# Optimization experiments

Hardware: AMD Instinct MI355X
Metric: run time of the kernel (lower is better)

The kernel has to match this reference:

```python
import math
import jax, jax.numpy as jnp
import numpy as np

NUM_HEAD = 16

def get_slopes(n):
    def pow2(n):
        start = 2 ** (-2 ** (-(math.log2(n) - 3)))
        return [start * start ** i for i in range(n)]
    if math.log2(n).is_integer():
        return pow2(n)
    c = 2 ** math.floor(math.log2(n))
    return pow2(c) + get_slopes(2 * c)[0::2][: n - c]

def setup_inputs() -> dict:
    key = jax.random.key(0)
    ks = jax.random.split(key, 9)
    B, T, C = 2, 2048, 2048
    x = jax.random.normal(ks[0], (B, T, C), dtype=jnp.float32)
    std = 0.02
    Wq = std * jax.random.normal(ks[1], (C, C), dtype=jnp.float32)
    Wk = std * jax.random.normal(ks[2], (C, C), dtype=jnp.float32)
    Wv = std * jax.random.normal(ks[3], (C, C), dtype=jnp.float32)
    Wo = (0.02 / np.sqrt(2 * 24)) * jax.random.normal(ks[4], (C, C), dtype=jnp.float32)
    bq = jnp.zeros((C,), jnp.float32)
    bk = jnp.zeros((C,), jnp.float32)
    bv = jnp.zeros((C,), jnp.float32)
    bo = jnp.zeros((C,), jnp.float32)
    return {"x": x, "Wq": Wq, "bq": bq, "Wk": Wk, "bk": bk,
            "Wv": Wv, "bv": bv, "Wo": Wo, "bo": bo}

def reference(x, Wq, bq, Wk, bk, Wv, bv, Wo, bo):
    B, T, C = x.shape
    H = NUM_HEAD
    D = C // H
    slopes = jnp.asarray(get_slopes(H), dtype=jnp.float32)  # [H]

    def split_heads(y):  # [B,T,C] -> [B,H,T,D]
        return y.reshape(B, T, H, D).transpose(0, 2, 1, 3)

    q = split_heads(x @ Wq + bq)
    k = split_heads(x @ Wk + bk)
    v = split_heads(x @ Wv + bv)

    attn = jnp.einsum("bhqd,bhkd->bhqk", q, k) / jnp.sqrt(jnp.float32(D))
    # ALiBi: bias[h, j] = slopes[h] * (j - (T-1)), broadcast over queries
    alibi = slopes[:, None, None] * (jnp.arange(T, dtype=jnp.float32) - (T - 1))[None, None, :]
    attn = attn + alibi  # [B,H,T,T] + [H,1,T]

    causal = jnp.tril(jnp.ones((T, T), dtype=bool))[None, None]
    attn = jnp.where(causal, attn, jnp.finfo(jnp.float32).min)
    p = jax.nn.softmax(attn, axis=-1)

    o = jnp.einsum("bhqk,bhkd->bhqd", p, v).transpose(0, 2, 1, 3).reshape(B, T, C)
    return o @ Wo + bo
```

## Files before the change

### kernel.cpp

```cpp
#include <hip/hip_runtime.h>
#include <math.h>


typedef unsigned short u16;
using bf16x8 = __attribute__((ext_vector_type(8))) short;
using f32x4  = __attribute__((ext_vector_type(4))) float;

__device__ __forceinline__ u16 f2bf(float f) {
  union { float f; unsigned u; } c; c.f = f;
  unsigned r = c.u + 0x7fffu + ((c.u >> 16) & 1u);
  return (u16)(r >> 16);
}
__device__ __forceinline__ float bf2f(u16 b) {
  union { unsigned u; float f; } c; c.u = ((unsigned)b) << 16; return c.f;
}
__device__ __forceinline__ unsigned cvtpk(float a, float b) {
  unsigned r;
  asm("v_cvt_pk_bf16_f32 %0, %1, %2" : "=v"(r) : "v"(a), "v"(b));
  return r;
}
__device__ __forceinline__ void g2l16(const void* g, void* l) {
  __builtin_amdgcn_global_load_lds(
      (const __attribute__((address_space(1))) void*)g,
      (__attribute__((address_space(3))) void*)l, 16, 0, 0);
}

__device__ __forceinline__ int band_jmin(int s, float slope2) {
  const int idist = (int)(36.0f / slope2);
  const int cut = 64 * s - idist - 31;
  return (cut > 0) ? (cut >> 5) : 0;
}

__device__ const unsigned char uord[48] = {
  15, 16, 32, 17, 33, 14, 18, 34, 19, 35,
  13, 20, 36, 21, 37, 12, 22, 38, 23, 39,
  11, 24, 40, 25, 41, 10, 26, 42, 27, 43,
   9, 28, 44, 29, 45,  8, 30, 46, 31, 47,
   7,  6,  5,  4,  3,  2,  1,  0};

__global__ __launch_bounds__(256) void split_f32(const float* __restrict__ in,
                                                 u16* __restrict__ hi, int n4) {
  for (int i = blockIdx.x * 256 + threadIdx.x; i < n4; i += gridDim.x * 256) {
    const float4 v = ((const float4*)in)[i];
    ushort4 h;
    h.x = f2bf(v.x); h.y = f2bf(v.y); h.z = f2bf(v.z); h.w = f2bf(v.w);
    ((ushort4*)hi)[i] = h;
  }
}

__global__ __launch_bounds__(256) void tsplit4_f32(
    const float* __restrict__ W0, const float* __restrict__ W1,
    const float* __restrict__ W2, const float* __restrict__ W3,
    u16* __restrict__ D0, u16* __restrict__ D1,
    u16* __restrict__ D2, u16* __restrict__ D3,
    int N, int K, float sc0) {
  __shared__ float tile[64][68];
  const int z = blockIdx.z;
  const float* W = (z == 0) ? W0 : (z == 1) ? W1 : (z == 2) ? W2 : W3;
  u16* Wth = (z == 0) ? D0 : (z == 1) ? D1 : (z == 2) ? D2 : D3;
  const float sc = (z == 0) ? sc0 : 1.f;
  const int tid = threadIdx.x;
  const int k0 = blockIdx.y * 64, n0 = blockIdx.x * 64;
  const int rr = tid >> 4, cc = (tid & 15) * 4;
#pragma unroll
  for (int u = 0; u < 4; ++u) {
    const float4 v = *(const float4*)&W[(size_t)(k0 + rr + 16 * u) * N + n0 + cc];
    tile[rr + 16 * u][cc + 0] = v.x;
    tile[rr + 16 * u][cc + 1] = v.y;
    tile[rr + 16 * u][cc + 2] = v.z;
    tile[rr + 16 * u][cc + 3] = v.w;
  }
  __syncthreads();
#pragma unroll
  for (int u = 0; u < 4; ++u) {
    const int nn = rr + 16 * u;
    ushort4 h;
    h.x = f2bf(tile[cc + 0][nn] * sc);
    h.y = f2bf(tile[cc + 1][nn] * sc);
    h.z = f2bf(tile[cc + 2][nn] * sc);
    h.w = f2bf(tile[cc + 3][nn] * sc);
    *(ushort4*)&Wth[(size_t)(n0 + nn) * K + k0 + cc] = h;
  }
}

template <int MODE>
__global__ __launch_bounds__(512, 4) void gemm256x128(
    const u16* __restrict__ Ah, const u16* __restrict__ Bth,
    const float* __restrict__ bias, const float* __restrict__ bias2,
    float bsc, u16* __restrict__ outH, u16* __restrict__ outH2,
    float* __restrict__ outF, int MM, int NN, int KK) {
  __shared__ u16 LA[3][8192];
  __shared__ u16 LB[3][4096];

  const int tid = threadIdx.x;
  const int wave = tid >> 6, lane = tid & 63;
  const int g = lane >> 4, q15 = lane & 15;
  const int wr = wave >> 1, wc = wave & 1;
  const int m0 = blockIdx.y * 256, n0 = blockIdx.x * 128;
  const int NT = KK >> 5;
  const int sxg = ((g ^ ((q15 >> 1) & 3)) << 4);

  f32x4 acc[4][4];
#pragma unroll
  for (int f = 0; f < 4; ++f)
#pragma unroll
    for (int j = 0; j < 4; ++j) acc[f][j] = (f32x4){0.f, 0.f, 0.f, 0.f};

  auto stageA = [&](int t, int rbuf) {
#pragma unroll
    for (int l = 0; l < 2; ++l) {
      const int ch = l * 512 + tid;
      const int row = ch >> 2, slot = ch & 3;
      const size_t ga = (size_t)(m0 + row) * KK + t * 32 +
                        ((slot ^ ((row >> 1) & 3)) * 8);
      g2l16(Ah + ga, (char*)(LA[rbuf]) + ch * 16);
    }
  };
  auto stageB = [&](int t, int rbuf) {
    const int ch = tid;
    const int row = ch >> 2, slot = ch & 3;
    const size_t gb = (size_t)(n0 + row) * KK + t * 32 +
                      ((slot ^ ((row >> 1) & 3)) * 8);
    g2l16(Bth + gb, (char*)(LB[rbuf]) + ch * 16);
  };

  stageA(0, 0); stageB(0, 0);
  __builtin_amdgcn_sched_barrier(0);
  if (NT > 1) { stageA(1, 1); stageB(1, 1); }
  __builtin_amdgcn_sched_barrier(0);
  if (NT > 1) { asm volatile("s_waitcnt vmcnt(3)" ::: "memory"); }
  else        { asm volatile("s_waitcnt vmcnt(0)" ::: "memory"); }
  __builtin_amdgcn_sched_barrier(0);
  __builtin_amdgcn_s_barrier();

  int rb = 0, rb2 = 2;
  for (int t = 0; t < NT; ++t) {
    const char* baseA = (const char*)(LA[rb]);
    const char* baseB = (const char*)(LB[rb]);

    bf16x8 af[4], bf[4];
#pragma unroll
    for (int f = 0; f < 4; ++f)
      af[f] = *(const bf16x8*)(baseA + (wr * 64 + f * 16 + q15) * 64 + sxg);
#pragma unroll
    for (int j = 0; j < 4; ++j)
      bf[j] = *(const bf16x8*)(baseB + (wc * 64 + j * 16 + q15) * 64 + sxg);
    if (t + 2 < NT) { stageA(t + 2, rb2); stageB(t + 2, rb2); }
    __builtin_amdgcn_sched_barrier(0);
    __builtin_amdgcn_s_barrier();
    asm volatile("s_waitcnt lgkmcnt(0)" ::: "memory");
    __builtin_amdgcn_sched_barrier(0);
    __builtin_amdgcn_s_setprio(1);
#pragma unroll
    for (int f = 0; f < 4; ++f)
#pragma unroll
      for (int j = 0; j < 4; ++j)
        acc[f][j] = __builtin_amdgcn_mfma_f32_16x16x32_bf16(
            af[f], bf[j], acc[f][j], 0, 0, 0);
    __builtin_amdgcn_s_setprio(0);
    if (t + 1 < NT) {
      if (t + 2 < NT) { asm volatile("s_waitcnt vmcnt(3)" ::: "memory"); }
      else            { asm volatile("s_waitcnt vmcnt(0)" ::: "memory"); }
    }
    __builtin_amdgcn_sched_barrier(0);
    __builtin_amdgcn_s_barrier();
    rb  = (rb  == 2) ? 0 : rb  + 1;
    rb2 = (rb2 == 2) ? 0 : rb2 + 1;
  }

#pragma unroll
  for (int f = 0; f < 4; ++f)
#pragma unroll
    for (int j = 0; j < 4; ++j)
#pragma unroll
      for (int r = 0; r < 4; ++r) {
        const int row = m0 + wr * 64 + f * 16 + g * 4 + r;
        const int col = n0 + wc * 64 + j * 16 + q15;
        const float v = acc[f][j][r];
        if (MODE == 0) {
          outF[(size_t)row * NN + col] = v + bias[col] * bsc;
        } else if (MODE == 2) {
          outH[(size_t)row * NN + col] = f2bf(v + bias[row] * bsc);
        } else {
          const int sel = col >> 11;
          const int c2 = col & 2047;
          const float vv = v + (sel ? bias2[c2] : bias[c2] * bsc);
          const int bb = row >> 11, tt = row & 2047;
          const int hh = c2 >> 7, dd = c2 & 127;
          (sel ? outH2 : outH)[(((size_t)bb * 16 + hh) * 2048 + tt) * 128 + dd] =
              f2bf(vv);
        }
      }
}

__global__ __launch_bounds__(64) void attn_splitk(
    const u16* __restrict__ Qh, const u16* __restrict__ Kh,
    const u16* __restrict__ Vth, u16* __restrict__ Oh,
    float* __restrict__ Obuf, float* __restrict__ mArr,
    float* __restrict__ lArr, int T, int NB, int BH) {
  __shared__ u16 KS[3][4096];

  const int tid = threadIdx.x;
  const int lane = tid & 63;
  const int g = lane >> 4, q15 = lane & 15;
  const int L = blockIdx.x;
  const int LL = (L & 7) | ((L >> 4) << 3);
  const int wid = (L >> 3) & 1;

  int bh, u;
  if (BH == 32) {
    const int k = LL >> 8;
    const int c = LL & 255;
    bh = (c + 5 * k) & 31;
    u = uord[k * 8 + (c >> 5)];
  } else {
    bh = LL / 48;
    u = uord[LL % 48];
  }
  int s, half;
  if (u < 16)      { s = u;      half = 2; }
  else if (u < 32) { s = 47 - u; half = 0; }
  else             { s = 63 - u; half = 1; }

  const int b = bh >> 4, h = bh & 15;
  const float slope2 = exp2f(-0.5f * (float)(h + 1)) * 1.44269504f;
  const int jmin = band_jmin(s, slope2);
  const bool loEmpty = (jmin >= s + 1);

  if (half == 0 && loEmpty) return;

  int lo, hi;
  if (half == 2)      { lo = jmin;                hi = 2 * s + 2; }
  else if (half == 0) { lo = jmin;                hi = s + 1; }
  else                { lo = loEmpty ? jmin : (s + 1); hi = 2 * s + 2; }
  const int ns = hi - lo;
  const bool maskable = (half != 0);
  const bool normStore = (half == 2) || (half == 1 && loEmpty);

  const int qw0 = s * 64 + wid * 32;
  const size_t vrow0 = (size_t)h * 128;
  const size_t vcol0 = (size_t)b * T;
  const size_t kbase = (size_t)bh * T;

  bf16x8 qfr[2][4];
#pragma unroll
  for (int qf2 = 0; qf2 < 2; ++qf2) {
    const size_t rb = ((size_t)bh * T + qw0 + qf2 * 16 + q15) * 128;
#pragma unroll
    for (int ks = 0; ks < 4; ++ks)
      qfr[qf2][ks] = *(const bf16x8*)&Qh[rb + ks * 32 + g * 8];
  }

  f32x4 oacc[2][8];
#pragma unroll
  for (int a = 0; a < 2; ++a)
#pragma unroll
    for (int n = 0; n < 8; ++n) oacc[a][n] = (f32x4){0.f, 0.f, 0.f, 0.f};
  float m_st[2] = {-1e5f, -1e5f};
  float l_part[2] = {0.f, 0.f};

  auto stageK = [&](int jt, int bf) {
    const int j0 = jt * 32;
#pragma unroll
    for (int c = 0; c < 8; ++c) {
      const int row = c * 4 + g;
      const int off = (q15 * 16) ^ ((row & 7) << 4);
      const size_t gb = (kbase + j0 + row) * 128;
      g2l16((const char*)(Kh + gb) + off, (char*)(KS[bf]) + c * 1024);
    }
  };
  auto loadV = [&](int jt, bf16x8 (&vf)[8]) {
    const int j0 = jt * 32;
#pragma unroll
    for (int nf = 0; nf < 8; ++nf)
      vf[nf] = *(const bf16x8*)
          &Vth[(vrow0 + nf * 16 + q15) * (size_t)NB + vcol0 + j0 + g * 8];
  };

  bf16x8 vfA[8], vfB[8];
  __builtin_amdgcn_sched_barrier(0);
  stageK(hi - 1, 0);
  if (ns > 1) stageK(hi - 2, 1);
  __builtin_amdgcn_sched_barrier(0);
  loadV(hi - 1, vfA);
  if (ns > 1) { asm volatile("s_waitcnt vmcnt(16)" ::: "memory"); }
  else        { asm volatile("s_waitcnt vmcnt(8)"  ::: "memory"); }
  __builtin_amdgcn_sched_barrier(0);

  int cur = 0;

  auto ITER = [&](int it, bf16x8 (&vc)[8], bf16x8 (&vn)[8]) {
    const int jt = hi - 1 - it;
    const int j0 = jt * 32;

    const bool haveV1 = (it + 1 < ns);
    const bool haveK2 = (it + 2 < ns);
    if (haveV1) loadV(jt - 1, vn);
    if (haveK2) {
      int nb = cur + 2; if (nb >= 3) nb -= 3;
      stageK(jt - 2, nb);
    }
    __builtin_amdgcn_sched_barrier(0);

    f32x4 sacc[2][2];
#pragma unroll
    for (int jf = 0; jf < 2; ++jf)
#pragma unroll
      for (int qf2 = 0; qf2 < 2; ++qf2) sacc[jf][qf2] = (f32x4){0.f, 0.f, 0.f, 0.f};
    __builtin_amdgcn_s_setprio(1);
#pragma unroll
    for (int ks = 0; ks < 4; ++ks) {
      bf16x8 ka[2];
#pragma unroll
      for (int jf = 0; jf < 2; ++jf) {
        const int row = jf * 16 + q15;
        const int off = (row * 256 + ks * 64 + g * 16) ^ ((row & 7) << 4);
        ka[jf] = *(const bf16x8*)((const char*)(KS[cur]) + off);
      }
#pragma unroll
      for (int jf = 0; jf < 2; ++jf)
#pragma unroll
        for (int qf2 = 0; qf2 < 2; ++qf2)
          sacc[jf][qf2] = __builtin_amdgcn_mfma_f32_16x16x32_bf16(
              ka[jf], qfr[qf2][ks], sacc[jf][qf2], 0, 0, 0);
    }
    __builtin_amdgcn_s_setprio(0);

    const float jb2 = (float)(j0 + 4 * g - (T - 1));

    unsigned Fw[2][4];
#pragma unroll
    for (int qf2 = 0; qf2 < 2; ++qf2) {
      const int qg = qw0 + qf2 * 16 + q15;
      float sv[2][4];
      float mt = -1e30f;
#pragma unroll
      for (int jf = 0; jf < 2; ++jf)
#pragma unroll
        for (int r = 0; r < 4; ++r) {
          float x = fmaf(slope2, jb2 + (float)(jf * 16 + r), sacc[jf][qf2][r]);
          if (maskable && it < 2) {
            const int jg = j0 + jf * 16 + 4 * g + r;
            x = (jg > qg) ? -1e30f : x;
          }
          sv[jf][r] = x;
          mt = fmaxf(mt, x);
        }
      if (!__all(mt <= m_st[qf2] + 11.0f)) {
        mt = fmaxf(mt, __shfl_xor(mt, 16));
        mt = fmaxf(mt, __shfl_xor(mt, 32));
        const float mnew = fmaxf(m_st[qf2], mt);
        const float scl = exp2f(m_st[qf2] - mnew);
        l_part[qf2] *= scl;
        m_st[qf2] = mnew;
#pragma unroll
        for (int r = 0; r < 4; ++r) {
          const float sc = __shfl(scl, g * 4 + r);
#pragma unroll
          for (int nf = 0; nf < 8; ++nf) oacc[qf2][nf][r] *= sc;
        }
      }
      float rs = 0.f;
      float p[2][4];
#pragma unroll
      for (int jf = 0; jf < 2; ++jf)
#pragma unroll
        for (int r = 0; r < 4; ++r) {
          p[jf][r] = exp2f(sv[jf][r] - m_st[qf2]);
          rs += p[jf][r];
        }
      l_part[qf2] += rs;
      const unsigned W00 = cvtpk(p[0][0], p[0][1]), W01 = cvtpk(p[0][2], p[0][3]);
      const unsigned W10 = cvtpk(p[1][0], p[1][1]), W11 = cvtpk(p[1][2], p[1][3]);
      const int srcA = q15 + ((g & 1) << 5);
      const int srcB = srcA + 16;
      const unsigned A0 = (unsigned)__shfl((int)W00, srcA);
      const unsigned A1 = (unsigned)__shfl((int)W01, srcA);
      const unsigned B0 = (unsigned)__shfl((int)W00, srcB);
      const unsigned B1 = (unsigned)__shfl((int)W01, srcB);
      const unsigned C0 = (unsigned)__shfl((int)W10, srcA);
      const unsigned C1 = (unsigned)__shfl((int)W11, srcA);
      const unsigned D0 = (unsigned)__shfl((int)W10, srcB);
      const unsigned D1 = (unsigned)__shfl((int)W11, srcB);
      const bool hi2 = g >= 2;
      Fw[qf2][0] = hi2 ? C0 : A0;
      Fw[qf2][1] = hi2 ? C1 : A1;
      Fw[qf2][2] = hi2 ? D0 : B0;
      Fw[qf2][3] = hi2 ? D1 : B1;
    }

    if (haveV1) {
      if (haveK2) { asm volatile("s_waitcnt vmcnt(16)" ::: "memory"); }
      else        { asm volatile("s_waitcnt vmcnt(8)"  ::: "memory"); }
    } else        { asm volatile("s_waitcnt vmcnt(0)"  ::: "memory"); }
    __builtin_amdgcn_sched_barrier(0);

    union { unsigned uu[4]; bf16x8 v; } pa0, pa1;
#pragma unroll
    for (int w = 0; w < 4; ++w) { pa0.uu[w] = Fw[0][w]; pa1.uu[w] = Fw[1][w]; }
    __builtin_amdgcn_s_setprio(1);
#pragma unroll
    for (int nf = 0; nf < 8; ++nf) {
      oacc[0][nf] = __builtin_amdgcn_mfma_f32_16x16x32_bf16(pa0.v, vc[nf], oacc[0][nf], 0, 0, 0);
      oacc[1][nf] = __builtin_amdgcn_mfma_f32_16x16x32_bf16(pa1.v, vc[nf], oacc[1][nf], 0, 0, 0);
    }
    __builtin_amdgcn_s_setprio(0);

    cur = (cur == 2) ? 0 : cur + 1;
  };

  for (int it = 0; it < ns;) {
    ITER(it, vfA, vfB); ++it;
    if (it >= ns) break;
    ITER(it, vfB, vfA); ++it;
  }

  float lrow[2];
#pragma unroll
  for (int qf2 = 0; qf2 < 2; ++qf2) {
    float lr = l_part[qf2];
    lr += __shfl_xor(lr, 16);
    lr += __shfl_xor(lr, 32);
    lrow[qf2] = lr;
  }

  if (normStore) {
#pragma unroll
    for (int qf2 = 0; qf2 < 2; ++qf2) {
      const float inv = 1.0f / lrow[qf2];
#pragma unroll
      for (int r = 0; r < 4; ++r) {
        const float iv = __shfl(inv, g * 4 + r);
        const int qrow = qw0 + qf2 * 16 + g * 4 + r;
        const size_t ob = ((size_t)b * T + qrow) * 2048 + h * 128;
#pragma unroll
        for (int nf = 0; nf < 8; ++nf)
          Oh[ob + nf * 16 + q15] = f2bf(oacc[qf2][nf][r] * iv);
      }
    }
  } else {
    const int sp = s - 16;
    const size_t sbase = ((size_t)(bh * 16 + sp) * 2 + half) * 64;
    if (g == 0) {
#pragma unroll
      for (int qf2 = 0; qf2 < 2; ++qf2) {
        mArr[sbase + wid * 32 + qf2 * 16 + q15] = m_st[qf2];
        lArr[sbase + wid * 32 + qf2 * 16 + q15] = lrow[qf2];
      }
    }
    const size_t obase = sbase * 128;
#pragma unroll
    for (int qf2 = 0; qf2 < 2; ++qf2)
#pragma unroll
      for (int r = 0; r < 4; ++r) {
        const int row = wid * 32 + qf2 * 16 + g * 4 + r;
#pragma unroll
        for (int nf = 0; nf < 8; ++nf)
          Obuf[obase + (size_t)row * 128 + nf * 16 + q15] = oacc[qf2][nf][r];
      }
  }
}

__global__ __launch_bounds__(128) void combine_halves(
    const float* __restrict__ Obuf, const float* __restrict__ mArr,
    const float* __restrict__ lArr, u16* __restrict__ Oh, int T) {
  const int idx = blockIdx.x;
  const int row = idx & 63;
  const int sp = (idx >> 6) & 15;
  const int bh = idx >> 10;
  const int d = threadIdx.x;
  const int s = sp + 16;
  const int b = bh >> 4, h = bh & 15;
  const float slope2 = exp2f(-0.5f * (float)(h + 1)) * 1.44269504f;
  if (band_jmin(s, slope2) >= s + 1) return;
  const size_t sbase = ((size_t)(bh * 16 + sp) * 2) * 64;
  const float m1 = mArr[sbase + row],      l1 = lArr[sbase + row];
  const float m2 = mArr[sbase + 64 + row], l2 = lArr[sbase + 64 + row];
  const float M = fmaxf(m1, m2);
  const float w1 = exp2f(m1 - M), w2 = exp2f(m2 - M);
  const float inv = 1.0f / (l1 * w1 + l2 * w2);
  const size_t ob = sbase * 128;
  const float o1 = Obuf[ob + (size_t)row * 128 + d];
  const float o2 = Obuf[ob + 8192 + (size_t)row * 128 + d];
  const float v = (o1 * w1 + o2 * w2) * inv;
  const int qrow = s * 64 + row;
  Oh[((size_t)b * T + qrow) * 2048 + h * 128 + d] = f2bf(v);
}

#define TM 128
#define BKG 8

template <int QKV>
__global__ __launch_bounds__(256) void gemm_f32(
    const float* __restrict__ A, const float* __restrict__ W,
    const float* __restrict__ bias, float* __restrict__ out,
    int M, int N, int K, int T) {
  __shared__ float As[BKG][TM];
  __shared__ float Bs[BKG][TM];
  const int tid = threadIdx.x;
  const int tx = tid & 15, ty = tid >> 4;
  const int m0 = blockIdx.y * TM, n0 = blockIdx.x * TM;
  float acc[8][8];
#pragma unroll
  for (int i = 0; i < 8; ++i)
#pragma unroll
    for (int j = 0; j < 8; ++j) acc[i][j] = 0.f;
  const int arow = tid >> 1, acol = (tid & 1) * 4;
  const int brow = tid >> 5, bcol = (tid & 31) * 4;
  for (int k0 = 0; k0 < K; k0 += BKG) {
    const float4 av = *(const float4*)&A[(size_t)(m0 + arow) * K + k0 + acol];
    const float4 bv = *(const float4*)&W[(size_t)(k0 + brow) * N + n0 + bcol];
    __syncthreads();
    As[acol + 0][arow] = av.x; As[acol + 1][arow] = av.y;
    As[acol + 2][arow] = av.z; As[acol + 3][arow] = av.w;
    *(float4*)&Bs[brow][bcol] = bv;
    __syncthreads();
#pragma unroll
    for (int kk = 0; kk < BKG; ++kk) {
      const float4 a0 = *(const float4*)&As[kk][ty * 4];
      const float4 a1 = *(const float4*)&As[kk][64 + ty * 4];
      const float4 b0 = *(const float4*)&Bs[kk][tx * 4];
      const float4 b1 = *(const float4*)&Bs[kk][64 + tx * 4];
      const float af[8] = {a0.x, a0.y, a0.z, a0.w, a1.x, a1.y, a1.z, a1.w};
      const float bf[8] = {b0.x, b0.y, b0.z, b0.w, b1.x, b1.y, b1.z, b1.w};
#pragma unroll
      for (int i = 0; i < 8; ++i)
#pragma unroll
        for (int j = 0; j < 8; ++j) acc[i][j] += af[i] * bf[j];
    }
  }
#pragma unroll
  for (int a = 0; a < 2; ++a)
#pragma unroll
    for (int i = 0; i < 4; ++i) {
      const int row = m0 + a * 64 + ty * 4 + i;
      const int bb = row / T, t = row % T;
#pragma unroll
      for (int bj = 0; bj < 2; ++bj) {
        const int col = n0 + bj * 64 + tx * 4;
        float4 r;
        r.x = acc[a * 4 + i][bj * 4 + 0] + bias[col + 0];
        r.y = acc[a * 4 + i][bj * 4 + 1] + bias[col + 1];
        r.z = acc[a * 4 + i][bj * 4 + 2] + bias[col + 2];
        r.w = acc[a * 4 + i][bj * 4 + 3] + bias[col + 3];
        if (QKV) {
          const int hh = col >> 7, dd = col & 127;
          *(float4*)&out[(((size_t)bb * 16 + hh) * T + t) * 128 + dd] = r;
        } else {
          *(float4*)&out[(size_t)row * N + col] = r;
        }
      }
    }
}

#define QT 32
#define KT 32
#define DP 132

__global__ __launch_bounds__(256) void flash_f32(
    const float* __restrict__ Q, const float* __restrict__ K,
    const float* __restrict__ V, float* __restrict__ O, int T) {
  __shared__ float Qs[QT][DP];
  __shared__ float Ks[KT][DP];
  __shared__ float Vs[KT][DP];
  __shared__ float Ps[QT][KT + 1];
  const int tid = threadIdx.x;
  const int jh = tid & 15, ih = tid >> 4;
  const int bh = blockIdx.y;
  const int h = bh & 15;
  const int q0 = blockIdx.x * QT;
  const float slope = exp2f(-0.5f * (float)(h + 1));
  const float rsD = 0.08838834764831845f;
  {
    const float* Qg = Q + ((size_t)bh * T + q0) * 128;
    const int r = tid >> 3, p = tid & 7;
#pragma unroll
    for (int u = 0; u < 4; ++u)
      *(float4*)&Qs[r][(p + 8 * u) * 4] = *(const float4*)&Qg[r * 128 + (p + 8 * u) * 4];
  }
  float m_st[2] = {-1e30f, -1e30f};
  float l_st[2] = {0.f, 0.f};
  float accv[2][8] = {};
  const int ktiles = blockIdx.x + 1;
  for (int kt = 0; kt < ktiles; ++kt) {
    const int j0 = kt * KT;
    const float* Kg = K + ((size_t)bh * T + j0) * 128;
    const float* Vg = V + ((size_t)bh * T + j0) * 128;
    __syncthreads();
    {
      const int r = tid >> 3, p = tid & 7;
#pragma unroll
      for (int u = 0; u < 4; ++u) {
        *(float4*)&Ks[r][(p + 8 * u) * 4] = *(const float4*)&Kg[r * 128 + (p + 8 * u) * 4];
        *(float4*)&Vs[r][(p + 8 * u) * 4] = *(const float4*)&Vg[r * 128 + (p + 8 * u) * 4];
      }
    }
    __syncthreads();
    float s00 = 0.f, s01 = 0.f, s10 = 0.f, s11 = 0.f;
#pragma unroll 8
    for (int d4 = 0; d4 < 32; ++d4) {
      const float4 qa = *(const float4*)&Qs[2 * ih + 0][4 * d4];
      const float4 qb = *(const float4*)&Qs[2 * ih + 1][4 * d4];
      const float4 ka = *(const float4*)&Ks[2 * jh + 0][4 * d4];
      const float4 kb = *(const float4*)&Ks[2 * jh + 1][4 * d4];
      s00 += qa.x * ka.x + qa.y * ka.y + qa.z * ka.z + qa.w * ka.w;
      s01 += qa.x * kb.x + qa.y * kb.y + qa.z * kb.z + qa.w * kb.w;
      s10 += qb.x * ka.x + qb.y * ka.y + qb.z * ka.z + qb.w * ka.w;
      s11 += qb.x * kb.x + qb.y * kb.y + qb.z * kb.z + qb.w * kb.w;
    }
    float sc[2][2] = {{s00, s01}, {s10, s11}};
    float mt[2];
#pragma unroll
    for (int r = 0; r < 2; ++r) {
      const int qg = q0 + 2 * ih + r;
#pragma unroll
      for (int c = 0; c < 2; ++c) {
        const int jg = j0 + 2 * jh + c;
        const float svv = sc[r][c] * rsD + slope * (float)(jg - (T - 1));
        sc[r][c] = (jg > qg) ? -1e30f : svv;
      }
      mt[r] = fmaxf(sc[r][0], sc[r][1]);
    }
#pragma unroll
    for (int m = 1; m < 16; m <<= 1) {
      mt[0] = fmaxf(mt[0], __shfl_xor(mt[0], m));
      mt[1] = fmaxf(mt[1], __shfl_xor(mt[1], m));
    }
#pragma unroll
    for (int r = 0; r < 2; ++r) {
      const float mnew = fmaxf(m_st[r], mt[r]);
      const float scl = (m_st[r] > -1e29f) ? expf(m_st[r] - mnew) : 0.f;
      const float p0 = expf(sc[r][0] - mnew);
      const float p1 = expf(sc[r][1] - mnew);
      float rs = p0 + p1;
#pragma unroll
      for (int m = 1; m < 16; m <<= 1) rs += __shfl_xor(rs, m);
      l_st[r] = l_st[r] * scl + rs;
      m_st[r] = mnew;
#pragma unroll
      for (int d = 0; d < 8; ++d) accv[r][d] *= scl;
      Ps[2 * ih + r][2 * jh + 0] = p0;
      Ps[2 * ih + r][2 * jh + 1] = p1;
    }
    __syncthreads();
#pragma unroll 4
    for (int j = 0; j < KT; ++j) {
      const float p0 = Ps[2 * ih + 0][j];
      const float p1 = Ps[2 * ih + 1][j];
      const float4 v0 = *(const float4*)&Vs[j][8 * jh];
      const float4 v1 = *(const float4*)&Vs[j][8 * jh + 4];
      accv[0][0] += p0 * v0.x; accv[0][1] += p0 * v0.y;
      accv[0][2] += p0 * v0.z; accv[0][3] += p0 * v0.w;
      accv[0][4] += p0 * v1.x; accv[0][5] += p0 * v1.y;
      accv[0][6] += p0 * v1.z; accv[0][7] += p0 * v1.w;
      accv[1][0] += p1 * v0.x; accv[1][1] += p1 * v0.y;
      accv[1][2] += p1 * v0.z; accv[1][3] += p1 * v0.w;
      accv[1][4] += p1 * v1.x; accv[1][5] += p1 * v1.y;
      accv[1][6] += p1 * v1.z; accv[1][7] += p1 * v1.w;
    }
  }
  const int b = bh >> 4;
#pragma unroll
  for (int r = 0; r < 2; ++r) {
    const int qg = q0 + 2 * ih + r;
    const float inv = 1.0f / l_st[r];
    float4 o0, o1;
    o0.x = accv[r][0] * inv; o0.y = accv[r][1] * inv;
    o0.z = accv[r][2] * inv; o0.w = accv[r][3] * inv;
    o1.x = accv[r][4] * inv; o1.y = accv[r][5] * inv;
    o1.z = accv[r][6] * inv; o1.w = accv[r][7] * inv;
    float* dst = O + ((size_t)b * T + qg) * 2048 + h * 128 + 8 * jh;
    *(float4*)&dst[0] = o0;
    *(float4*)&dst[4] = o1;
  }
}

extern "C" void kernel_launch(void* const* d_in, const int* in_sizes, int n_in,
                              void* d_out, int out_size, void* d_ws,
                              size_t ws_size, hipStream_t stream) {
  const float* x  = (const float*)d_in[0];
  const float* Wq = (const float*)d_in[1];
  const float* bq = (const float*)d_in[2];
  const float* Wk = (const float*)d_in[3];
  const float* bk = (const float*)d_in[4];
  const float* Wv = (const float*)d_in[5];
  const float* bv = (const float*)d_in[6];
  const float* Wo = (const float*)d_in[7];
  const float* bo = (const float*)d_in[8];
  float* out = (float*)d_out;

  const int C = 2048, T = 2048, H = 16;
  const int M = in_sizes[0] / C;
  const int B = M / T;
  const int BH = B * H;
  const size_t MC = (size_t)M * C, CC = (size_t)C * C;
  const size_t splitO = (size_t)BH * 16 * 2 * 8192;
  const size_t splitML = (size_t)BH * 16 * 2 * 64;
  const size_t need = (5 * MC + 4 * CC) * sizeof(u16) +
                      (splitO + 2 * splitML) * sizeof(float);

  const float QSC = 0.08838834764831845f * 1.44269504088896f;

  if (ws_size >= need && (M % 256) == 0) {
    u16* p = (u16*)d_ws;
    u16* xh   = p; p += MC;
    u16* wqth = p; p += CC;
    u16* wkth = p; p += CC;
    u16* wvth = p; p += CC;
    u16* woth = p; p += CC;
    u16* qh   = p; p += MC;
    u16* kh   = p; p += MC;
    u16* vth  = p; p += MC;
    u16* oh   = p; p += MC;
    float* Obuf = (float*)p;
    float* mArr = Obuf + splitO;
    float* lArr = mArr + splitML;

    split_f32<<<1024, 256, 0, stream>>>(x, xh, (int)(MC / 4));
    dim3 tg(C / 64, C / 64, 4);
    tsplit4_f32<<<tg, 256, 0, stream>>>(Wq, Wk, Wv, Wo, wqth, wkth, wvth,
                                        woth, C, C, QSC);

    dim3 gqk(2 * C / 128, M / 256);
    gemm256x128<3><<<gqk, 512, 0, stream>>>(xh, wqth, bq, bk, QSC, qh, kh,
                                            nullptr, M, 2 * C, C);
    dim3 gv(M / 128, C / 256);
    gemm256x128<2><<<gv, 512, 0, stream>>>(wvth, xh, bv, nullptr, 1.f, vth,
                                           nullptr, nullptr, C, M, C);

    attn_splitk<<<96 * BH, 64, 0, stream>>>(qh, kh, vth, oh, Obuf, mArr,
                                            lArr, T, M, BH);
    combine_halves<<<BH * 16 * 64, 128, 0, stream>>>(Obuf, mArr, lArr, oh, T);

    dim3 gq(C / 128, M / 256);
    gemm256x128<0><<<gq, 512, 0, stream>>>(oh, woth, bo, nullptr, 1.f,
                                           nullptr, nullptr, out, M, C, C);
  } else {
    float* Qw = (float*)d_ws;
    float* Kw = Qw + MC;
    float* Vw = Kw + MC;
    float* Ow = Vw + MC;
    dim3 ggrid(C / TM, M / TM);
    gemm_f32<1><<<ggrid, 256, 0, stream>>>(x, Wq, bq, Qw, M, C, C, T);
    gemm_f32<1><<<ggrid, 256, 0, stream>>>(x, Wk, bk, Kw, M, C, C, T);
    gemm_f32<1><<<ggrid, 256, 0, stream>>>(x, Wv, bv, Vw, M, C, C, T);
    dim3 fgrid(T / QT, B * H);
    flash_f32<<<fgrid, 256, 0, stream>>>(Qw, Kw, Vw, Ow, T);
    gemm_f32<0><<<ggrid, 256, 0, stream>>>(Ow, Wo, bo, out, M, C, C, T);
  }
}
```

Before: 283.9 us.

## Load K tiles directly into registers instead of staging through LDS

Removes the triple-buffered LDS staging of K (global_load_lds plus swizzled LDS reads) and instead loads K fragments from global memory straight into registers, double-buffered alongside V. The wait for the next tile's loads now sits at the start of each iteration, before the QK MFMAs, rather than before the PV MFMAs. This drops the LDS traffic and LDS footprint but raises register pressure, cuts K prefetch depth from two tiles to one, and exposes more global-load latency before the QK product.

```diff
diff --git a/kernel.cpp b/kernel.cpp
--- a/kernel.cpp
+++ b/kernel.cpp
@@ -198,8 +198,6 @@
     const u16* __restrict__ Vth, u16* __restrict__ Oh,
     float* __restrict__ Obuf, float* __restrict__ mArr,
     float* __restrict__ lArr, int T, int NB, int BH) {
-  __shared__ u16 KS[3][4096];
-
   const int tid = threadIdx.x;
   const int lane = tid & 63;
   const int g = lane >> 4, q15 = lane & 15;
@@ -259,14 +257,14 @@
   float m_st[2] = {-1e5f, -1e5f};
   float l_part[2] = {0.f, 0.f};
 
-  auto stageK = [&](int jt, int bf) {
+  auto loadK = [&](int jt, bf16x8 (&kf)[2][4]) {
     const int j0 = jt * 32;
 #pragma unroll
-    for (int c = 0; c < 8; ++c) {
-      const int row = c * 4 + g;
-      const int off = (q15 * 16) ^ ((row & 7) << 4);
-      const size_t gb = (kbase + j0 + row) * 128;
-      g2l16((const char*)(Kh + gb) + off, (char*)(KS[bf]) + c * 1024);
+    for (int jf = 0; jf < 2; ++jf) {
+      const size_t rbk = (kbase + j0 + jf * 16 + q15) * 128;
+#pragma unroll
+      for (int ks = 0; ks < 4; ++ks)
+        kf[jf][ks] = *(const bf16x8*)&Kh[rbk + ks * 32 + g * 8];
     }
   };
   auto loadV = [&](int jt, bf16x8 (&vf)[8]) {
@@ -277,29 +275,22 @@
           &Vth[(vrow0 + nf * 16 + q15) * (size_t)NB + vcol0 + j0 + g * 8];
   };
 
-  bf16x8 vfA[8], vfB[8];
+  bf16x8 kfA[2][4], kfB[2][4], vfA[8], vfB[8];
   __builtin_amdgcn_sched_barrier(0);
-  stageK(hi - 1, 0);
-  if (ns > 1) stageK(hi - 2, 1);
+  loadK(hi - 1, kfA);
+  loadV(hi - 1, vfA);
   __builtin_amdgcn_sched_barrier(0);
-  loadV(hi - 1, vfA);
-  if (ns > 1) { asm volatile("s_waitcnt vmcnt(16)" ::: "memory"); }
-  else        { asm volatile("s_waitcnt vmcnt(8)"  ::: "memory"); }
-  __builtin_amdgcn_sched_barrier(0);
-
-  int cur = 0;
-
-  auto ITER = [&](int it, bf16x8 (&vc)[8], bf16x8 (&vn)[8]) {
+
+  auto ITER = [&](int it, bf16x8 (&kc)[2][4], bf16x8 (&vc)[8],
+                  bf16x8 (&kn)[2][4], bf16x8 (&vn)[8]) {
     const int jt = hi - 1 - it;
     const int j0 = jt * 32;
 
-    const bool haveV1 = (it + 1 < ns);
-    const bool haveK2 = (it + 2 < ns);
-    if (haveV1) loadV(jt - 1, vn);
-    if (haveK2) {
-      int nb = cur + 2; if (nb >= 3) nb -= 3;
-      stageK(jt - 2, nb);
-    }
+    const bool haveN = (it + 1 < ns);
+    if (haveN) { loadK(jt - 1, kn); loadV(jt - 1, vn); }
+    __builtin_amdgcn_sched_barrier(0);
+    if (haveN) { asm volatile("s_waitcnt vmcnt(16)" ::: "memory"); }
+    else       { asm volatile("s_waitcnt vmcnt(0)"  ::: "memory"); }
     __builtin_amdgcn_sched_barrier(0);
 
     f32x4 sacc[2][2];
@@ -309,21 +300,13 @@
       for (int qf2 = 0; qf2 < 2; ++qf2) sacc[jf][qf2] = (f32x4){0.f, 0.f, 0.f, 0.f};
     __builtin_amdgcn_s_setprio(1);
 #pragma unroll
-    for (int ks = 0; ks < 4; ++ks) {
-      bf16x8 ka[2];
-#pragma unroll
-      for (int jf = 0; jf < 2; ++jf) {
-        const int row = jf * 16 + q15;
-        const int off = (row * 256 + ks * 64 + g * 16) ^ ((row & 7) << 4);
-        ka[jf] = *(const bf16x8*)((const char*)(KS[cur]) + off);
-      }
+    for (int ks = 0; ks < 4; ++ks)
 #pragma unroll
       for (int jf = 0; jf < 2; ++jf)
 #pragma unroll
         for (int qf2 = 0; qf2 < 2; ++qf2)
           sacc[jf][qf2] = __builtin_amdgcn_mfma_f32_16x16x32_bf16(
-              ka[jf], qfr[qf2][ks], sacc[jf][qf2], 0, 0, 0);
-    }
+              kc[jf][ks], qfr[qf2][ks], sacc[jf][qf2], 0, 0, 0);
     __builtin_amdgcn_s_setprio(0);
 
     const float jb2 = (float)(j0 + 4 * g - (T - 1));
@@ -389,12 +372,6 @@
       Fw[qf2][3] = hi2 ? D1 : B1;
     }
 
-    if (haveV1) {
-      if (haveK2) { asm volatile("s_waitcnt vmcnt(16)" ::: "memory"); }
-      else        { asm volatile("s_waitcnt vmcnt(8)"  ::: "memory"); }
-    } else        { asm volatile("s_waitcnt vmcnt(0)"  ::: "memory"); }
-    __builtin_amdgcn_sched_barrier(0);
-
     union { unsigned uu[4]; bf16x8 v; } pa0, pa1;
 #pragma unroll
     for (int w = 0; w < 4; ++w) { pa0.uu[w] = Fw[0][w]; pa1.uu[w] = Fw[1][w]; }
@@ -405,14 +382,12 @@
       oacc[1][nf] = __builtin_amdgcn_mfma_f32_16x16x32_bf16(pa1.v, vc[nf], oacc[1][nf], 0, 0, 0);
     }
     __builtin_amdgcn_s_setprio(0);
-
-    cur = (cur == 2) ? 0 : cur + 1;
   };
 
   for (int it = 0; it < ns;) {
-    ITER(it, vfA, vfB); ++it;
+    ITER(it, kfA, vfA, kfB, vfB); ++it;
     if (it >= ns) break;
-    ITER(it, vfB, vfA); ++it;
+    ITER(it, kfB, vfB, kfA, vfA); ++it;
   }
 
   float lrow[2];
```

New measurement: 297.2 us. 4.7% more time.

## Pair attention iterations to batch two QK^T tiles before softmax-PV

Applied to the files above, without the earlier changes.

Restructures the flash-attention inner loop to process two KV tiles per step. Both QK^T MFMA blocks are issued back-to-back, and the V/K prefetches and waitcnts are reshuffled around the two softmax+PV phases. The aim is to give the scheduler more independent MFMA work to hide softmax latency and memory waits. It costs extra accumulator registers, which may hurt occupancy, and it changes the ordering of the triple-buffered K slots.

```diff
diff --git a/kernel.cpp b/kernel.cpp
--- a/kernel.cpp
+++ b/kernel.cpp
@@ -276,38 +276,11 @@
       vf[nf] = *(const bf16x8*)
           &Vth[(vrow0 + nf * 16 + q15) * (size_t)NB + vcol0 + j0 + g * 8];
   };
-
-  bf16x8 vfA[8], vfB[8];
-  __builtin_amdgcn_sched_barrier(0);
-  stageK(hi - 1, 0);
-  if (ns > 1) stageK(hi - 2, 1);
-  __builtin_amdgcn_sched_barrier(0);
-  loadV(hi - 1, vfA);
-  if (ns > 1) { asm volatile("s_waitcnt vmcnt(16)" ::: "memory"); }
-  else        { asm volatile("s_waitcnt vmcnt(8)"  ::: "memory"); }
-  __builtin_amdgcn_sched_barrier(0);
-
-  int cur = 0;
-
-  auto ITER = [&](int it, bf16x8 (&vc)[8], bf16x8 (&vn)[8]) {
-    const int jt = hi - 1 - it;
-    const int j0 = jt * 32;
-
-    const bool haveV1 = (it + 1 < ns);
-    const bool haveK2 = (it + 2 < ns);
-    if (haveV1) loadV(jt - 1, vn);
-    if (haveK2) {
-      int nb = cur + 2; if (nb >= 3) nb -= 3;
-      stageK(jt - 2, nb);
-    }
-    __builtin_amdgcn_sched_barrier(0);
-
-    f32x4 sacc[2][2];
+  auto QKT = [&](int slot, f32x4 (&sacc)[2][2]) {
 #pragma unroll
     for (int jf = 0; jf < 2; ++jf)
 #pragma unroll
       for (int qf2 = 0; qf2 < 2; ++qf2) sacc[jf][qf2] = (f32x4){0.f, 0.f, 0.f, 0.f};
-    __builtin_amdgcn_s_setprio(1);
 #pragma unroll
     for (int ks = 0; ks < 4; ++ks) {
       bf16x8 ka[2];
@@ -315,7 +288,7 @@
       for (int jf = 0; jf < 2; ++jf) {
         const int row = jf * 16 + q15;
         const int off = (row * 256 + ks * 64 + g * 16) ^ ((row & 7) << 4);
-        ka[jf] = *(const bf16x8*)((const char*)(KS[cur]) + off);
+        ka[jf] = *(const bf16x8*)((const char*)(KS[slot]) + off);
       }
 #pragma unroll
       for (int jf = 0; jf < 2; ++jf)
@@ -324,10 +297,9 @@
           sacc[jf][qf2] = __builtin_amdgcn_mfma_f32_16x16x32_bf16(
               ka[jf], qfr[qf2][ks], sacc[jf][qf2], 0, 0, 0);
     }
-    __builtin_amdgcn_s_setprio(0);
-
+  };
+  auto SOFTPV = [&](int it, int j0, f32x4 (&sacc)[2][2], bf16x8 (&vc)[8]) {
     const float jb2 = (float)(j0 + 4 * g - (T - 1));
-
     unsigned Fw[2][4];
 #pragma unroll
     for (int qf2 = 0; qf2 < 2; ++qf2) {
@@ -388,13 +360,6 @@
       Fw[qf2][2] = hi2 ? D0 : B0;
       Fw[qf2][3] = hi2 ? D1 : B1;
     }
-
-    if (haveV1) {
-      if (haveK2) { asm volatile("s_waitcnt vmcnt(16)" ::: "memory"); }
-      else        { asm volatile("s_waitcnt vmcnt(8)"  ::: "memory"); }
-    } else        { asm volatile("s_waitcnt vmcnt(0)"  ::: "memory"); }
-    __builtin_amdgcn_sched_barrier(0);
-
     union { unsigned uu[4]; bf16x8 v; } pa0, pa1;
 #pragma unroll
     for (int w = 0; w < 4; ++w) { pa0.uu[w] = Fw[0][w]; pa1.uu[w] = Fw[1][w]; }
@@ -405,14 +370,66 @@
       oacc[1][nf] = __builtin_amdgcn_mfma_f32_16x16x32_bf16(pa1.v, vc[nf], oacc[1][nf], 0, 0, 0);
     }
     __builtin_amdgcn_s_setprio(0);
-
-    cur = (cur == 2) ? 0 : cur + 1;
   };
 
-  for (int it = 0; it < ns;) {
-    ITER(it, vfA, vfB); ++it;
-    if (it >= ns) break;
-    ITER(it, vfB, vfA); ++it;
+  bf16x8 vfA[8], vfB[8];
+  __builtin_amdgcn_sched_barrier(0);
+  stageK(hi - 1, 0);
+  if (ns > 1) stageK(hi - 2, 1);
+  __builtin_amdgcn_sched_barrier(0);
+  loadV(hi - 1, vfA);
+  if (ns > 1) { asm volatile("s_waitcnt vmcnt(16)" ::: "memory"); }
+  else        { asm volatile("s_waitcnt vmcnt(8)"  ::: "memory"); }
+  __builtin_amdgcn_sched_barrier(0);
+
+  int cur = 0;
+
+  int it = 0;
+  while (it + 2 <= ns) {
+    const int jt0 = hi - 1 - it, jt1 = jt0 - 1;
+    const int j0a = jt0 * 32, j0b = jt1 * 32;
+    const int cur1 = (cur == 2) ? 0 : cur + 1;
+    const int cur2 = (cur1 == 2) ? 0 : cur1 + 1;
+    const bool e2 = (it + 2 < ns);
+    const bool e3 = (it + 3 < ns);
+
+    loadV(jt1, vfB);
+    if (e2) stageK(jt0 - 2, cur2);
+    __builtin_amdgcn_sched_barrier(0);
+    if (e2) { asm volatile("s_waitcnt vmcnt(16)" ::: "memory"); }
+    else    { asm volatile("s_waitcnt vmcnt(8)"  ::: "memory"); }
+    __builtin_amdgcn_sched_barrier(0);
+
+    f32x4 sacc0[2][2], sacc1[2][2];
+    __builtin_amdgcn_s_setprio(1);
+    QKT(cur, sacc0);
+    QKT(cur1, sacc1);
+    __builtin_amdgcn_s_setprio(0);
+
+    SOFTPV(it, j0a, sacc0, vfA);
+
+    if (e2) loadV(jt0 - 2, vfA);
+    if (e3) stageK(jt0 - 3, cur);
+    __builtin_amdgcn_sched_barrier(0);
+    if (e2 && e3)      { asm volatile("s_waitcnt vmcnt(16)" ::: "memory"); }
+    else if (e2)       { asm volatile("s_waitcnt vmcnt(8)"  ::: "memory"); }
+    else               { asm volatile("s_waitcnt vmcnt(0)"  ::: "memory"); }
+    __builtin_amdgcn_sched_barrier(0);
+
+    SOFTPV(it + 1, j0b, sacc1, vfB);
+
+    cur = cur2;
+    it += 2;
+  }
+  if (it < ns) {
+    const int jt = hi - 1 - it;
+    asm volatile("s_waitcnt vmcnt(0)" ::: "memory");
+    __builtin_amdgcn_sched_barrier(0);
+    f32x4 sacc0[2][2];
+    __builtin_amdgcn_s_setprio(1);
+    QKT(cur, sacc0);
+    __builtin_amdgcn_s_setprio(0);
+    SOFTPV(it, jt * 32, sacc0, vfA);
   }
 
   float lrow[2];
```

Result: no change. 280.6 us, median of 2 (-1.2%).
